# Kernel optimization log

Measured on AMD Instinct MI355X. Metric: run time of the kernel, lower is better.

## Reference

```python
import jax, jax.numpy as jnp
import numpy as np


def setup_inputs() -> dict:
    key = jax.random.key(0)
    ks = jax.random.split(key, 7)
    B, D, T, H = 32, 512, 4096, 512
    return {
        "query": jax.random.normal(ks[0], (B, D, 1), dtype=jnp.float32),
        "keys": jax.random.normal(ks[1], (B, D, T), dtype=jnp.float32),
        "values": jax.random.normal(ks[2], (B, D, T), dtype=jnp.float32),
        "w42": 0.01 * jax.random.normal(ks[3], (H, 2 * D), dtype=jnp.float32),
        "b4": 0.01 * jax.random.normal(ks[4], (H, 1), dtype=jnp.float32),
        "w54": 0.01 * jax.random.normal(ks[5], (1, H), dtype=jnp.float32),
        "b5": 0.01 * jax.random.normal(ks[6], (1, 1), dtype=jnp.float32),
    }


def reference(query, keys, values, w42, b4, w54, b5):
    D = keys.shape[1]
    # cat([keys, query.repeat T], dim=1) then w42 @ cat ==
    # w42[:, :D] @ keys + w42[:, D:] @ query (broadcast over T)
    n4 = (jnp.einsum('hd,bdt->bht', w42[:, :D], keys)
          + jnp.einsum('hd,bdo->bho', w42[:, D:], query)  # [B,H,1], broadcasts over T
          + b4)                                            # [H,1] broadcasts
    a4 = jnp.tanh(n4)                                      # [B,H,T]
    n5 = jnp.einsum('oh,bht->bot', w54, a4) + b5           # [B,1,T]
    # transpose(1,2) -> [B,T,1], softmax over dim=1 (T)
    a5 = jax.nn.softmax(n5[:, 0, :], axis=-1)              # [B,T]
    a6 = jnp.einsum('bvt,bt->bv', values, a5)[..., None]   # [B,Dv,1]
    return a6
```

## Files before the change

### kernel.cpp

```cpp
#include <hip/hip_runtime.h>
#include <hip/hip_bf16.h>
#include <cstdint>
#include <cstddef>

typedef __attribute__((ext_vector_type(4))) float f32x4;
typedef __attribute__((ext_vector_type(8))) short s16x8;
typedef __attribute__((ext_vector_type(4))) unsigned short u16x4;
typedef __attribute__((ext_vector_type(8))) unsigned short u16x8;

#define NB 32
#define DD 512
#define TT 4096
#define HH 512
#define TB 64
#define BK 32
#define NKK 16

__device__ __forceinline__ unsigned short f2bf(float f) {
  uint32_t u = __builtin_bit_cast(uint32_t, f);
  u += 0x7fffu + ((u >> 16) & 1u);
  return (unsigned short)(u >> 16);
}

__device__ __forceinline__ float tanh_fast(float x) {
  x = fminf(fmaxf(x, -15.f), 15.f);
  float e = __expf(2.f * x);
  return (e - 1.f) / (e + 1.f);
}

__global__ void kConvT(const float* __restrict__ w42, u16x8* __restrict__ W1swz) {
  int g = blockIdx.x * 256 + threadIdx.x;
  int h = g & 511, sk = g >> 9;
  int kk = sk >> 2, s = sk & 3;
  const float* src = &w42[h * 1024 + kk * 32 + s * 8];
  f32x4 v0 = *reinterpret_cast<const f32x4*>(src);
  f32x4 v1 = *reinterpret_cast<const f32x4*>(src + 4);
  u16x8 c;
  c[0] = f2bf(v0.x); c[1] = f2bf(v0.y); c[2] = f2bf(v0.z); c[3] = f2bf(v0.w);
  c[4] = f2bf(v1.x); c[5] = f2bf(v1.y); c[6] = f2bf(v1.z); c[7] = f2bf(v1.w);
  W1swz[kk * 2048 + s * 512 + h] = c;
}

__global__ void kQterm(const float* __restrict__ w42, const float* __restrict__ query,
                       const float* __restrict__ b4, float* __restrict__ qterm) {
  int wid = blockIdx.x * 4 + (threadIdx.x >> 6);
  int lane = threadIdx.x & 63;
  int b = wid >> 9, h = wid & 511;
  const float* wr = &w42[h * 1024 + 512];
  const float* q  = &query[b * 512];
  int d = lane * 8;
  f32x4 w0 = *(const f32x4*)&wr[d], w1 = *(const f32x4*)&wr[d + 4];
  f32x4 q0 = *(const f32x4*)&q[d],  q1 = *(const f32x4*)&q[d + 4];
  float s = w0.x*q0.x + w0.y*q0.y + w0.z*q0.z + w0.w*q0.w
          + w1.x*q1.x + w1.y*q1.y + w1.z*q1.z + w1.w*q1.w;
  #pragma unroll
  for (int off = 32; off; off >>= 1) s += __shfl_xor(s, off);
  if (lane == 0) qterm[b * 512 + h] = s + b4[h];
}

__global__ __launch_bounds__(256, 2) void kMain(
    const float* __restrict__ keys, const u16x8* __restrict__ W1swz,
    const float* __restrict__ qterm, const float* __restrict__ w54,
    float* __restrict__ n5) {
  __shared__ s16x8 Bs[2 * 4 * 64];
  __shared__ float red[4][64];

  int bid = blockIdx.x;
  int b = bid >> 6, tblk = bid & 63;
  int t0 = tblk * TB;
  int tid = threadIdx.x, lane = tid & 63, w = tid >> 6;
  int lr = lane & 15, lg = lane >> 4;

  const float* kp = keys + (size_t)b * DD * TT + (size_t)(w * 8) * TT + t0 + lane;
  const s16x8* ap = reinterpret_cast<const s16x8*>(W1swz) + lg * 512 + w * 128 + lr;

  f32x4 acc[8][4];
  #pragma unroll
  for (int m = 0; m < 8; ++m)
    #pragma unroll
    for (int n = 0; n < 4; ++n) acc[m][n] = (f32x4){0.f, 0.f, 0.f, 0.f};

  float r[8];
  #pragma unroll
  for (int j = 0; j < 8; ++j) r[j] = kp[(size_t)j * TT];

  for (int kk = 0; kk < NKK; ++kk) {
    s16x8 c;
    #pragma unroll
    for (int j = 0; j < 8; ++j) c[j] = (short)f2bf(r[j]);
    Bs[((kk & 1) * 4 + w) * 64 + lane] = c;

    s16x8 af[8];
    #pragma unroll
    for (int m = 0; m < 8; ++m) af[m] = ap[kk * 2048 + m * 16];

    if (kk + 1 < NKK) {
      const float* kp2 = kp + (size_t)(kk + 1) * BK * TT;
      #pragma unroll
      for (int j = 0; j < 8; ++j) r[j] = kp2[(size_t)j * TT];
    }

    asm volatile("s_waitcnt lgkmcnt(0)" ::: "memory");
    __builtin_amdgcn_s_barrier();

    s16x8 bf[4];
    #pragma unroll
    for (int n = 0; n < 4; ++n)
      bf[n] = Bs[((kk & 1) * 4 + lg) * 64 + n * 16 + lr];

    #pragma unroll
    for (int m = 0; m < 8; ++m)
      #pragma unroll
      for (int n = 0; n < 4; ++n)
        acc[m][n] = __builtin_amdgcn_mfma_f32_16x16x32_bf16(af[m], bf[n], acc[m][n], 0, 0, 0);
  }

  float part[4] = {0.f, 0.f, 0.f, 0.f};
  int hb = w * 128;
  #pragma unroll
  for (int m = 0; m < 8; ++m) {
    #pragma unroll
    for (int rr = 0; rr < 4; ++rr) {
      int h = hb + m * 16 + lg * 4 + rr;
      float qv = qterm[b * HH + h];
      float wv = w54[h];
      #pragma unroll
      for (int n = 0; n < 4; ++n)
        part[n] += wv * tanh_fast(acc[m][n][rr] + qv);
    }
  }
  #pragma unroll
  for (int n = 0; n < 4; ++n) {
    part[n] += __shfl_xor(part[n], 16);
    part[n] += __shfl_xor(part[n], 32);
  }
  if (lane < 16) {
    #pragma unroll
    for (int n = 0; n < 4; ++n) red[w][n * 16 + lane] = part[n];
  }
  __syncthreads();
  if (tid < 64) {
    float v = red[0][tid] + red[1][tid] + red[2][tid] + red[3][tid];
    n5[b * TT + t0 + tid] = v;
  }
}

__global__ void kSoftmax(const float* __restrict__ n5, float* __restrict__ a5) {
  int b = blockIdx.x, tid = threadIdx.x;
  int lane = tid & 63, wid = tid >> 6;
  __shared__ float sm[4];
  __shared__ float ssum[4];
  float vals[16];
  float mx = -1e30f;
  #pragma unroll
  for (int i = 0; i < 16; ++i) {
    float v = n5[b * TT + tid + i * 256];
    vals[i] = v; mx = fmaxf(mx, v);
  }
  #pragma unroll
  for (int off = 32; off; off >>= 1) mx = fmaxf(mx, __shfl_xor(mx, off));
  if (lane == 0) sm[wid] = mx;
  __syncthreads();
  mx = fmaxf(fmaxf(sm[0], sm[1]), fmaxf(sm[2], sm[3]));
  float s = 0.f;
  #pragma unroll
  for (int i = 0; i < 16; ++i) { vals[i] = __expf(vals[i] - mx); s += vals[i]; }
  #pragma unroll
  for (int off = 32; off; off >>= 1) s += __shfl_xor(s, off);
  if (lane == 0) ssum[wid] = s;
  __syncthreads();
  s = ssum[0] + ssum[1] + ssum[2] + ssum[3];
  float inv = 1.f / s;
  #pragma unroll
  for (int i = 0; i < 16; ++i) a5[b * TT + tid + i * 256] = vals[i] * inv;
}

__global__ void kOut(const float* __restrict__ values, const float* __restrict__ a5,
                     float* __restrict__ out) {
  int blk = blockIdx.x;
  int b = blk >> 7;
  int wid = threadIdx.x >> 6, lane = threadIdx.x & 63;
  int v = (blk & 127) * 4 + wid;
  const float* row = &values[((size_t)b * 512 + v) * TT];
  const float* wv = &a5[b * TT];
  float s = 0.f;
  #pragma unroll
  for (int i = 0; i < 16; ++i) {
    int t = (i * 64 + lane) * 4;
    f32x4 x = *(const f32x4*)&row[t];
    f32x4 y = *(const f32x4*)&wv[t];
    s += x.x * y.x + x.y * y.y + x.z * y.z + x.w * y.w;
  }
  #pragma unroll
  for (int off = 32; off; off >>= 1) s += __shfl_xor(s, off);
  if (lane == 0) out[b * 512 + v] = s;
}

extern "C" void kernel_launch(void* const* d_in, const int* in_sizes, int n_in,
                              void* d_out, int out_size, void* d_ws, size_t ws_size,
                              hipStream_t stream) {
  const float* query  = (const float*)d_in[0];
  const float* keys   = (const float*)d_in[1];
  const float* values = (const float*)d_in[2];
  const float* w42    = (const float*)d_in[3];
  const float* b4     = (const float*)d_in[4];
  const float* w54    = (const float*)d_in[5];
  float* out = (float*)d_out;

  char* ws = (char*)d_ws;
  u16x8* W1swz = (u16x8*)ws;
  float* qterm = (float*)(ws + 524288);
  float* n5    = (float*)(ws + 524288 + 65536);
  float* a5    = (float*)(ws + 524288 + 65536 + 524288);

  kConvT  <<<128, 256, 0, stream>>>(w42, W1swz);
  kQterm  <<<4096, 256, 0, stream>>>(w42, query, b4, qterm);
  kMain   <<<2048, 256, 0, stream>>>(keys, W1swz, qterm, w54, n5);
  kSoftmax<<<32, 256, 0, stream>>>(n5, a5);
  kOut    <<<4096, 256, 0, stream>>>(values, a5, out);
}
```

Baseline: 167.7 us.

## Fuse softmax and value reduction into main kernel with deeper prefetch

The main kernel now exponentiates its scores per tile and writes per-tile partial sums of exp. It also immediately reads the matching values tile to write per-tile weighted partial outputs. A small final kernel sums the partials and normalizes, replacing the separate softmax and output kernels along with the n5/a5 round trips. The max subtraction is dropped, which relies on the scores staying bounded; that holds here because they are a tanh-weighted sum. The MFMA loop also double-buffers the weight fragments and prefetches keys two steps ahead, at the cost of more registers.

```diff
diff --git a/kernel.cpp b/kernel.cpp
--- a/kernel.cpp
+++ b/kernel.cpp
@@ -59,11 +59,12 @@
 }
 
 __global__ __launch_bounds__(256, 2) void kMain(
-    const float* __restrict__ keys, const u16x8* __restrict__ W1swz,
-    const float* __restrict__ qterm, const float* __restrict__ w54,
-    float* __restrict__ n5) {
+    const float* __restrict__ keys, const float* __restrict__ values,
+    const u16x8* __restrict__ W1swz, const float* __restrict__ qterm,
+    const float* __restrict__ w54, float* __restrict__ P, float* __restrict__ Zp) {
   __shared__ s16x8 Bs[2 * 4 * 64];
   __shared__ float red[4][64];
+  __shared__ float e_s[64];
 
   int bid = blockIdx.x;
   int b = bid >> 6, tblk = bid & 63;
@@ -80,24 +81,31 @@
     #pragma unroll
     for (int n = 0; n < 4; ++n) acc[m][n] = (f32x4){0.f, 0.f, 0.f, 0.f};
 
-  float r[8];
-  #pragma unroll
-  for (int j = 0; j < 8; ++j) r[j] = kp[(size_t)j * TT];
-
+  s16x8 af[2][8];
+  float r[2][8];
+  #pragma unroll
+  for (int m = 0; m < 8; ++m) af[0][m] = ap[m * 16];
+  #pragma unroll
+  for (int j = 0; j < 8; ++j) r[0][j] = kp[(size_t)j * TT];
+  #pragma unroll
+  for (int j = 0; j < 8; ++j) r[1][j] = kp[(size_t)(BK + j) * TT];
+
+  #pragma unroll
   for (int kk = 0; kk < NKK; ++kk) {
+    const int cur = kk & 1;
     s16x8 c;
     #pragma unroll
-    for (int j = 0; j < 8; ++j) c[j] = (short)f2bf(r[j]);
-    Bs[((kk & 1) * 4 + w) * 64 + lane] = c;
-
-    s16x8 af[8];
-    #pragma unroll
-    for (int m = 0; m < 8; ++m) af[m] = ap[kk * 2048 + m * 16];
+    for (int j = 0; j < 8; ++j) c[j] = (short)f2bf(r[cur][j]);
+    Bs[(cur * 4 + w) * 64 + lane] = c;
 
     if (kk + 1 < NKK) {
-      const float* kp2 = kp + (size_t)(kk + 1) * BK * TT;
-      #pragma unroll
-      for (int j = 0; j < 8; ++j) r[j] = kp2[(size_t)j * TT];
+      #pragma unroll
+      for (int m = 0; m < 8; ++m) af[cur ^ 1][m] = ap[(kk + 1) * 2048 + m * 16];
+    }
+    if (kk + 2 < NKK) {
+      const float* kp2 = kp + (size_t)(kk + 2) * BK * TT;
+      #pragma unroll
+      for (int j = 0; j < 8; ++j) r[cur][j] = kp2[(size_t)j * TT];
     }
 
     asm volatile("s_waitcnt lgkmcnt(0)" ::: "memory");
@@ -106,13 +114,13 @@
     s16x8 bf[4];
     #pragma unroll
     for (int n = 0; n < 4; ++n)
-      bf[n] = Bs[((kk & 1) * 4 + lg) * 64 + n * 16 + lr];
+      bf[n] = Bs[(cur * 4 + lg) * 64 + n * 16 + lr];
 
     #pragma unroll
     for (int m = 0; m < 8; ++m)
       #pragma unroll
       for (int n = 0; n < 4; ++n)
-        acc[m][n] = __builtin_amdgcn_mfma_f32_16x16x32_bf16(af[m], bf[n], acc[m][n], 0, 0, 0);
+        acc[m][n] = __builtin_amdgcn_mfma_f32_16x16x32_bf16(af[cur][m], bf[n], acc[m][n], 0, 0, 0);
   }
 
   float part[4] = {0.f, 0.f, 0.f, 0.f};
@@ -141,59 +149,52 @@
   __syncthreads();
   if (tid < 64) {
     float v = red[0][tid] + red[1][tid] + red[2][tid] + red[3][tid];
-    n5[b * TT + t0 + tid] = v;
-  }
-}
-
-__global__ void kSoftmax(const float* __restrict__ n5, float* __restrict__ a5) {
+    float e = __expf(v);
+    e_s[tid] = e;
+    float z = e;
+    #pragma unroll
+    for (int off = 32; off; off >>= 1) z += __shfl_xor(z, off);
+    if (tid == 0) Zp[b * 64 + tblk] = z;
+  }
+  __syncthreads();
+
+  f32x4 ee = *(const f32x4*)&e_s[lr * 4];
+  const float* vb = values + (size_t)b * DD * TT + t0 + lr * 4;
+  float* Pb = P + ((size_t)b * 64 + tblk) * 512;
+  int q = lane >> 4;
+  #pragma unroll 8
+  for (int it = 0; it < 32; ++it) {
+    int v = w * 128 + it * 4 + q;
+    f32x4 x = *(const f32x4*)&vb[(size_t)v * TT];
+    float s = x.x * ee.x + x.y * ee.y + x.z * ee.z + x.w * ee.w;
+    s += __shfl_xor(s, 1);
+    s += __shfl_xor(s, 2);
+    s += __shfl_xor(s, 4);
+    s += __shfl_xor(s, 8);
+    if (lr == 0) Pb[v] = s;
+  }
+}
+
+__global__ void kFinal(const float* __restrict__ P, const float* __restrict__ Zp,
+                       float* __restrict__ out) {
   int b = blockIdx.x, tid = threadIdx.x;
-  int lane = tid & 63, wid = tid >> 6;
-  __shared__ float sm[4];
-  __shared__ float ssum[4];
-  float vals[16];
-  float mx = -1e30f;
-  #pragma unroll
-  for (int i = 0; i < 16; ++i) {
-    float v = n5[b * TT + tid + i * 256];
-    vals[i] = v; mx = fmaxf(mx, v);
-  }
-  #pragma unroll
-  for (int off = 32; off; off >>= 1) mx = fmaxf(mx, __shfl_xor(mx, off));
-  if (lane == 0) sm[wid] = mx;
+  __shared__ float zsh;
+  if (tid < 64) {
+    float z = Zp[b * 64 + tid];
+    #pragma unroll
+    for (int off = 32; off; off >>= 1) z += __shfl_xor(z, off);
+    if (tid == 0) zsh = z;
+  }
   __syncthreads();
-  mx = fmaxf(fmaxf(sm[0], sm[1]), fmaxf(sm[2], sm[3]));
-  float s = 0.f;
-  #pragma unroll
-  for (int i = 0; i < 16; ++i) { vals[i] = __expf(vals[i] - mx); s += vals[i]; }
-  #pragma unroll
-  for (int off = 32; off; off >>= 1) s += __shfl_xor(s, off);
-  if (lane == 0) ssum[wid] = s;
-  __syncthreads();
-  s = ssum[0] + ssum[1] + ssum[2] + ssum[3];
-  float inv = 1.f / s;
-  #pragma unroll
-  for (int i = 0; i < 16; ++i) a5[b * TT + tid + i * 256] = vals[i] * inv;
-}
-
-__global__ void kOut(const float* __restrict__ values, const float* __restrict__ a5,
-                     float* __restrict__ out) {
-  int blk = blockIdx.x;
-  int b = blk >> 7;
-  int wid = threadIdx.x >> 6, lane = threadIdx.x & 63;
-  int v = (blk & 127) * 4 + wid;
-  const float* row = &values[((size_t)b * 512 + v) * TT];
-  const float* wv = &a5[b * TT];
-  float s = 0.f;
-  #pragma unroll
-  for (int i = 0; i < 16; ++i) {
-    int t = (i * 64 + lane) * 4;
-    f32x4 x = *(const f32x4*)&row[t];
-    f32x4 y = *(const f32x4*)&wv[t];
-    s += x.x * y.x + x.y * y.y + x.z * y.z + x.w * y.w;
-  }
-  #pragma unroll
-  for (int off = 32; off; off >>= 1) s += __shfl_xor(s, off);
-  if (lane == 0) out[b * 512 + v] = s;
+  float inv = 1.f / zsh;
+  float s0 = 0.f, s1 = 0.f;
+  const float* Pb = P + (size_t)b * 64 * 512;
+  for (int tile = 0; tile < 64; ++tile) {
+    s0 += Pb[tile * 512 + tid];
+    s1 += Pb[tile * 512 + 256 + tid];
+  }
+  out[b * 512 + tid] = s0 * inv;
+  out[b * 512 + 256 + tid] = s1 * inv;
 }
 
 extern "C" void kernel_launch(void* const* d_in, const int* in_sizes, int n_in,
@@ -209,13 +210,12 @@
 
   char* ws = (char*)d_ws;
   u16x8* W1swz = (u16x8*)ws;
-  float* qterm = (float*)(ws + 524288);
-  float* n5    = (float*)(ws + 524288 + 65536);
-  float* a5    = (float*)(ws + 524288 + 65536 + 524288);
-
-  kConvT  <<<128, 256, 0, stream>>>(w42, W1swz);
-  kQterm  <<<4096, 256, 0, stream>>>(w42, query, b4, qterm);
-  kMain   <<<2048, 256, 0, stream>>>(keys, W1swz, qterm, w54, n5);
-  kSoftmax<<<32, 256, 0, stream>>>(n5, a5);
-  kOut    <<<4096, 256, 0, stream>>>(values, a5, out);
-}
+  float* qterm = (float*)(ws + (512 << 10));
+  float* Zp    = (float*)(ws + (576 << 10));
+  float* P     = (float*)(ws + (1024 << 10));
+
+  kConvT <<<128, 256, 0, stream>>>(w42, W1swz);
+  kQterm <<<4096, 256, 0, stream>>>(w42, query, b4, qterm);
+  kMain  <<<2048, 256, 0, stream>>>(keys, values, W1swz, qterm, w54, P, Zp);
+  kFinal <<<32, 256, 0, stream>>>(P, Zp, out);
+}
```

After: 212.5 us. 1.27x slower.
